# Kernel optimization log

Measured on AMD Instinct MI355X. Metric: run time of the kernel, lower is better.

The kernel has to match this reference:

```python
import jax, jax.numpy as jnp
import numpy as np

EPS = 0.1
MAX_ITER = 100
THRESH = 0.1


def _M(C, u, v):
    # M_ij = (-C_ij + u_i + v_j) / eps  -> [B, N, Mp]
    return (-C + u[..., :, None] + v[..., None, :]) / EPS


def setup_inputs() -> dict:
    key = jax.random.key(0)
    k1, k2, k3 = jax.random.split(key, 3)
    x = jax.random.normal(k1, (16, 1024, 2), dtype=jnp.float32)
    y = jax.random.normal(k2, (16, 1024, 2), dtype=jnp.float32)
    C = jax.random.uniform(k3, (16, 1024, 1024), dtype=jnp.float32)
    return {"x": x, "y": y, "C": C}


def _sinkhorn(x, y, C):
    B = x.shape[0]
    N = x.shape[-2]
    Mp = y.shape[-2]
    mu = jnp.full((B, N), 1.0 / N, dtype=jnp.float32)
    nu = jnp.full((B, Mp), 1.0 / Mp, dtype=jnp.float32)
    log_mu = jnp.log(mu + 1e-8)
    log_nu = jnp.log(nu + 1e-8)

    u0 = jnp.zeros_like(mu)
    v0 = jnp.zeros_like(nu)

    def body(carry, _):
        u, v, done = carry
        u1 = u
        u_new = EPS * (log_mu - jax.nn.logsumexp(_M(C, u, v), axis=-1)) + u
        v_new = EPS * (log_nu - jax.nn.logsumexp(_M(C, u_new, v), axis=-2)) + v
        err = jnp.abs(u_new - u1).sum(-1).mean()
        # emulate torch's early break: freeze u,v once converged
        u = jnp.where(done, u, u_new)
        v = jnp.where(done, v, v_new)
        done = done | (err < THRESH)
        return (u, v, done), None

    (u, v, _), _ = jax.lax.scan(body, (u0, v0, jnp.array(False)), None, length=MAX_ITER)
    pi = jnp.exp(_M(C, u, v))                 # [B, N, Mp]
    cost = jnp.sum(pi * C, axis=(-2, -1))      # [B]
    return cost, pi


def reference(x, y, C):
    cost, pi = _sinkhorn(x, y, C)
    return (cost, pi, C)
```

## Files before the change

### kernel.cpp

```cpp
#include <hip/hip_runtime.h>
#include <hip/hip_fp16.h>

#define BB 16
#define NN 1024
#define MAX_ITER 100

constexpr float EPS_F    = 0.1f;
constexpr float INV_EPS  = 10.0f;
constexpr float MU_P     = 0.0009765625f + 1e-8f;
constexpr float LOG_MU   = -6.9314615656526045f;
constexpr float THRESH_B = 1.6f;

#define SCOPE_AGENT __HIP_MEMORY_SCOPE_AGENT

__device__ __forceinline__ float coh_loadf(float* p) {
    return __hip_atomic_load(p, __ATOMIC_RELAXED, SCOPE_AGENT);
}
__device__ __forceinline__ int coh_loadi(int* p) {
    return __hip_atomic_load(p, __ATOMIC_RELAXED, SCOPE_AGENT);
}
__device__ __forceinline__ void coh_storef(float* p, float v) {
    atomicExch(p, v);
}

__device__ __forceinline__ void batch_sync(int* cnt, int target) {
    __syncthreads();
    if (threadIdx.x == 0) {
        __threadfence_block();
        atomicAdd(cnt, 1);
        while (coh_loadi(cnt) < target) __builtin_amdgcn_s_sleep(1);
        __threadfence_block();
    }
    __syncthreads();
}

__global__ __launch_bounds__(256) void prep_kernel(
    const float* __restrict__ C, __half* __restrict__ E,
    float* __restrict__ u, float* __restrict__ wv,
    float* __restrict__ errB, float* __restrict__ errTot,
    int* __restrict__ errCnt, int* __restrict__ bsync)
{
    size_t gid = (size_t)blockIdx.x * 256 + threadIdx.x;
    float4 c = ((const float4*)C)[gid];
    __half2* E2 = (__half2*)E;
    E2[2*gid]   = __floats2half2_rn(__expf(-INV_EPS*c.x), __expf(-INV_EPS*c.y));
    E2[2*gid+1] = __floats2half2_rn(__expf(-INV_EPS*c.z), __expf(-INV_EPS*c.w));
    if (gid < BB*NN) { u[gid] = 0.f; wv[gid] = 1.f; }
    if (gid < 6400) errB[gid] = 0.f;
    if (gid < 400)  { errTot[gid] = 0.f; errCnt[gid] = 0; }
    if (gid < 256)  bsync[gid] = 0;
}

__global__ __launch_bounds__(1024, 4) void sink_iter(
    const __half* __restrict__ E, float* __restrict__ u, float* __restrict__ v,
    float* __restrict__ wv, float* __restrict__ Tpart,
    float* __restrict__ errB, float* __restrict__ errTot,
    int* __restrict__ errCnt, int* __restrict__ bsync)
{
    const int tid  = threadIdx.x;
    const int lane = tid & 63;
    const int wav  = tid >> 6;
    const int blk  = blockIdx.x;
    const int slot = blk >> 3;
    const int b    = ((blk & 7) << 1) | (slot >> 4);
    const int sub  = slot & 15;

    const __half* Eb = E + ((size_t)b << 20);
    float* ub  = u  + (b << 10);
    float* vb  = v  + (b << 10);
    float* wvb = wv + (b << 10);
    float* Tb  = Tpart + (b << 14);
    int*   bs  = bsync + (b << 4);

    __shared__ float part[16][1028];
    __shared__ float wv_lds[1024];
    __shared__ float werr[16];
    __shared__ float errv_s;

    for (int it = 0; it < MAX_ITER; ++it) {
        wv_lds[tid ^ (((tid >> 4) & 7) << 2)] = coh_loadf(&wvb[tid]);
        __syncthreads();

        float wf[16];
        #pragma unroll
        for (int j = 0; j < 4; ++j) {
            int idx = ((lane << 4) | (j << 2)) ^ ((lane & 7) << 2);
            float4 t4 = *(const float4*)&wv_lds[idx];
            wf[4*j+0] = t4.x; wf[4*j+1] = t4.y; wf[4*j+2] = t4.z; wf[4*j+3] = t4.w;
        }

        float acc[16];
        #pragma unroll
        for (int k = 0; k < 16; ++k) acc[k] = 0.f;
        float derr = 0.f;
        #pragma unroll
        for (int r = 0; r < 4; ++r) {
            const int row = (sub << 6) + (wav << 2) + r;
            const uint4* Ep = (const uint4*)(Eb + ((size_t)row << 10));
            union { uint4 q; __half2 h[4]; } a0, a1;
            a0.q = Ep[2*lane];
            a1.q = Ep[2*lane + 1];
            float f0[8], f1[8];
            #pragma unroll
            for (int k = 0; k < 4; ++k) {
                float2 fa = __half22float2(a0.h[k]);
                float2 fb = __half22float2(a1.h[k]);
                f0[2*k] = fa.x; f0[2*k+1] = fa.y;
                f1[2*k] = fb.x; f1[2*k+1] = fb.y;
            }
            float s = 0.f;
            #pragma unroll
            for (int k = 0; k < 8; ++k) s = fmaf(f0[k], wf[k], s);
            #pragma unroll
            for (int k = 0; k < 8; ++k) s = fmaf(f1[k], wf[8+k], s);
            #pragma unroll
            for (int off = 32; off >= 1; off >>= 1) s += __shfl_xor(s, off);
            float un = EPS_F * (LOG_MU - __logf(s));
            derr += fabsf(un - ub[row]);
            if (lane == 0) ub[row] = un;
            float wuv = MU_P / s;
            #pragma unroll
            for (int k = 0; k < 8; ++k) acc[k]   = fmaf(f0[k], wuv, acc[k]);
            #pragma unroll
            for (int k = 0; k < 8; ++k) acc[8+k] = fmaf(f1[k], wuv, acc[8+k]);
        }
        if (lane == 0) werr[wav] = derr;

        #pragma unroll
        for (int j = 0; j < 4; ++j) {
            int idx = ((lane << 4) | (j << 2)) ^ ((lane & 7) << 2);
            *(float4*)&part[wav][idx] =
                make_float4(acc[4*j], acc[4*j+1], acc[4*j+2], acc[4*j+3]);
        }
        __syncthreads();

        {
            int pidx = tid ^ (((tid >> 4) & 7) << 2);
            float ts = 0.f;
            #pragma unroll
            for (int w = 0; w < 16; ++w) ts += part[w][pidx];
            coh_storef(&Tb[(sub << 10) + tid], ts);
        }
        if (wav == 0) {
            float e = (lane < 16) ? werr[lane] : 0.f;
            #pragma unroll
            for (int off = 8; off >= 1; off >>= 1) e += __shfl_xor(e, off);
            if (lane == 0) atomicAdd(&errB[(((it << 4) + b) << 2)], e);
        }

        batch_sync(bs, (it << 5) + 16);

        if (sub == 0 && tid == 0) {
            float eb = coh_loadf(&errB[(((it << 4) + b) << 2)]);
            atomicAdd(&errTot[it << 2], eb);
            __threadfence_block();
            atomicAdd(&errCnt[it << 2], 1);
        }

        {
            const int s16 = tid >> 6;
            const int cl  = tid & 63;
            float pv = coh_loadf(&Tb[(s16 << 10) + (sub << 6) + cl]);
            part[s16][cl] = pv;
            __syncthreads();
            if (tid < 64) {
                float t = 0.f;
                #pragma unroll
                for (int w = 0; w < 16; ++w) t += part[w][tid];
                const int col = (sub << 6) + tid;
                vb[col] = EPS_F * (LOG_MU - __logf(t));
                coh_storef(&wvb[col], MU_P / t);
            }
        }

        batch_sync(bs, (it << 5) + 32);

        if (tid == 0) {
            while (coh_loadi(&errCnt[it << 2]) < 16) __builtin_amdgcn_s_sleep(1);
            errv_s = coh_loadf(&errTot[it << 2]);
        }
        __syncthreads();
        if (errv_s < THRESH_B) break;
    }
}

__global__ __launch_bounds__(256) void epilogue(
    const float* __restrict__ C, const float* __restrict__ u, const float* __restrict__ v,
    float* __restrict__ outPi, float* __restrict__ outC, float* __restrict__ part)
{
    int blk = blockIdx.x;
    int b = blk >> 10;
    int i = blk & 1023;
    size_t base = (size_t)blk << 10;
    const float4* C4 = (const float4*)(C + base);
    const float4* v4 = (const float4*)(v + ((size_t)b << 10));
    float4* P4 = (float4*)(outPi + base);
    float4* O4 = (float4*)(outC + base);
    float ui = u[(b << 10) + i];
    int t = threadIdx.x;
    float4 c = C4[t];
    float4 vv = v4[t];
    float4 p;
    p.x = __expf((ui + vv.x - c.x) * INV_EPS);
    p.y = __expf((ui + vv.y - c.y) * INV_EPS);
    p.z = __expf((ui + vv.z - c.z) * INV_EPS);
    p.w = __expf((ui + vv.w - c.w) * INV_EPS);
    P4[t] = p;
    O4[t] = c;
    float cp = p.x*c.x + p.y*c.y + p.z*c.z + p.w*c.w;
    #pragma unroll
    for (int off = 32; off >= 1; off >>= 1) cp += __shfl_xor(cp, off);
    __shared__ float ps[4];
    if ((t & 63) == 0) ps[t >> 6] = cp;
    __syncthreads();
    if (t == 0) part[blk] = ps[0] + ps[1] + ps[2] + ps[3];
}

__global__ __launch_bounds__(1024) void cost_reduce(
    const float* __restrict__ part, float* __restrict__ outCost)
{
    int b = blockIdx.x;
    int t = threadIdx.x;
    float s = part[(b << 10) + t];
    #pragma unroll
    for (int off = 32; off >= 1; off >>= 1) s += __shfl_xor(s, off);
    __shared__ float ps[16];
    if ((t & 63) == 0) ps[t >> 6] = s;
    __syncthreads();
    if (t < 64) {
        float e = (t < 16) ? ps[t] : 0.f;
        #pragma unroll
        for (int off = 8; off >= 1; off >>= 1) e += __shfl_xor(e, off);
        if (t == 0) outCost[b] = e;
    }
}

extern "C" void kernel_launch(void* const* d_in, const int* in_sizes, int n_in,
                              void* d_out, int out_size, void* d_ws, size_t ws_size,
                              hipStream_t stream)
{
    const float* C = (const float*)d_in[2];
    float* out = (float*)d_out;

    char* ws = (char*)d_ws;
    __half* E     = (__half*)ws;
    float* u      = (float*)(ws + (size_t)33554432);
    float* v      = u + 16384;
    float* wv     = v + 16384;
    float* part   = wv + 16384;
    float* errB   = part + 16384;
    float* errTot = errB + 6400;
    int*   errCnt = (int*)(errTot + 400);
    int*   bsync  = errCnt + 400;

    float* outPi = out + 16;
    float* outC  = out + 16 + (size_t)16777216;
    float* Tpart = outPi;

    prep_kernel<<<16384, 256, 0, stream>>>(C, E, u, wv, errB, errTot, errCnt, bsync);

    void* args[] = { (void*)&E, (void*)&u, (void*)&v, (void*)&wv, (void*)&Tpart,
                     (void*)&errB, (void*)&errTot, (void*)&errCnt, (void*)&bsync };
    hipLaunchCooperativeKernel((void*)sink_iter, dim3(256), dim3(1024),
                               args, 0, stream);

    epilogue<<<16384, 256, 0, stream>>>(C, u, v, outPi, outC, part);
    cost_reduce<<<16, 1024, 0, stream>>>(part, out);
}
```

Before: 253.7 us.

## Keep exp(-C/eps) tiles in registers and merge v-update into one barrier

Removes the prep kernel that wrote a half-precision exp(-C/eps) matrix to workspace. Each block now computes its own tile from C once and keeps it in registers across all iterations, so the loop no longer streams E from memory. The v update is made redundant per block: every block reads all 16 partial column sums from a double-buffered Tpart and computes wv locally, which drops the second grid barrier and the wv round-trip. u is kept in registers and written back only at the end, and the cost reduction kernel is replaced by atomics in the epilogue. The costs are higher register pressure, redundant reads of Tpart by every block, and a non-deterministic atomic summation order for the cost.

```diff
diff --git a/kernel.cpp b/kernel.cpp
--- a/kernel.cpp
+++ b/kernel.cpp
@@ -26,34 +26,23 @@
 __device__ __forceinline__ void batch_sync(int* cnt, int target) {
     __syncthreads();
     if (threadIdx.x == 0) {
-        __threadfence_block();
         atomicAdd(cnt, 1);
         while (coh_loadi(cnt) < target) __builtin_amdgcn_s_sleep(1);
-        __threadfence_block();
     }
     __syncthreads();
 }
 
-__global__ __launch_bounds__(256) void prep_kernel(
-    const float* __restrict__ C, __half* __restrict__ E,
-    float* __restrict__ u, float* __restrict__ wv,
-    float* __restrict__ errB, float* __restrict__ errTot,
-    int* __restrict__ errCnt, int* __restrict__ bsync)
-{
-    size_t gid = (size_t)blockIdx.x * 256 + threadIdx.x;
-    float4 c = ((const float4*)C)[gid];
-    __half2* E2 = (__half2*)E;
-    E2[2*gid]   = __floats2half2_rn(__expf(-INV_EPS*c.x), __expf(-INV_EPS*c.y));
-    E2[2*gid+1] = __floats2half2_rn(__expf(-INV_EPS*c.z), __expf(-INV_EPS*c.w));
-    if (gid < BB*NN) { u[gid] = 0.f; wv[gid] = 1.f; }
-    if (gid < 6400) errB[gid] = 0.f;
-    if (gid < 400)  { errTot[gid] = 0.f; errCnt[gid] = 0; }
-    if (gid < 256)  bsync[gid] = 0;
+__global__ __launch_bounds__(1024) void init_kernel(
+    int* __restrict__ ctrs, float* __restrict__ outCost)
+{
+    int gid = blockIdx.x * 1024 + threadIdx.x;
+    if (gid < 7456) ctrs[gid] = 0;
+    if (gid < BB)   outCost[gid] = 0.f;
 }
 
 __global__ __launch_bounds__(1024, 4) void sink_iter(
-    const __half* __restrict__ E, float* __restrict__ u, float* __restrict__ v,
-    float* __restrict__ wv, float* __restrict__ Tpart,
+    const float* __restrict__ C, float* __restrict__ u, float* __restrict__ v,
+    float* __restrict__ Tpart,
     float* __restrict__ errB, float* __restrict__ errTot,
     int* __restrict__ errCnt, int* __restrict__ bsync)
 {
@@ -65,11 +54,10 @@
     const int b    = ((blk & 7) << 1) | (slot >> 4);
     const int sub  = slot & 15;
 
-    const __half* Eb = E + ((size_t)b << 20);
-    float* ub  = u  + (b << 10);
-    float* vb  = v  + (b << 10);
-    float* wvb = wv + (b << 10);
-    float* Tb  = Tpart + (b << 14);
+    const float* Cb = C + ((size_t)b << 20);
+    float* ub  = u + (b << 10);
+    float* vb  = v + (b << 10);
+    float* Tb  = Tpart + (b << 15);
     int*   bs  = bsync + (b << 4);
 
     __shared__ float part[16][1028];
@@ -77,9 +65,32 @@
     __shared__ float werr[16];
     __shared__ float errv_s;
 
+    uint4 e[4][2];
+    #pragma unroll
+    for (int r = 0; r < 4; ++r) {
+        const float4* C4 = (const float4*)(
+            Cb + (((size_t)((sub << 6) + (wav << 2) + r)) << 10) + (lane << 4));
+        float4 c0 = C4[0], c1 = C4[1], c2 = C4[2], c3 = C4[3];
+        union { uint4 q; __half2 h[4]; } p0, p1;
+        p0.h[0] = __floats2half2_rn(__expf(-INV_EPS*c0.x), __expf(-INV_EPS*c0.y));
+        p0.h[1] = __floats2half2_rn(__expf(-INV_EPS*c0.z), __expf(-INV_EPS*c0.w));
+        p0.h[2] = __floats2half2_rn(__expf(-INV_EPS*c1.x), __expf(-INV_EPS*c1.y));
+        p0.h[3] = __floats2half2_rn(__expf(-INV_EPS*c1.z), __expf(-INV_EPS*c1.w));
+        p1.h[0] = __floats2half2_rn(__expf(-INV_EPS*c2.x), __expf(-INV_EPS*c2.y));
+        p1.h[1] = __floats2half2_rn(__expf(-INV_EPS*c2.z), __expf(-INV_EPS*c2.w));
+        p1.h[2] = __floats2half2_rn(__expf(-INV_EPS*c3.x), __expf(-INV_EPS*c3.y));
+        p1.h[3] = __floats2half2_rn(__expf(-INV_EPS*c3.z), __expf(-INV_EPS*c3.w));
+        e[r][0] = p0.q;
+        e[r][1] = p1.q;
+    }
+
+    float u_prev[4] = {0.f, 0.f, 0.f, 0.f};
+    float t_last = 1.0f;
+    wv_lds[tid] = 1.0f;
+    __syncthreads();
+
     for (int it = 0; it < MAX_ITER; ++it) {
-        wv_lds[tid ^ (((tid >> 4) & 7) << 2)] = coh_loadf(&wvb[tid]);
-        __syncthreads();
+        const int par = it & 1;
 
         float wf[16];
         #pragma unroll
@@ -95,34 +106,27 @@
         float derr = 0.f;
         #pragma unroll
         for (int r = 0; r < 4; ++r) {
-            const int row = (sub << 6) + (wav << 2) + r;
-            const uint4* Ep = (const uint4*)(Eb + ((size_t)row << 10));
             union { uint4 q; __half2 h[4]; } a0, a1;
-            a0.q = Ep[2*lane];
-            a1.q = Ep[2*lane + 1];
-            float f0[8], f1[8];
+            a0.q = e[r][0]; a1.q = e[r][1];
+            float f[16];
             #pragma unroll
             for (int k = 0; k < 4; ++k) {
                 float2 fa = __half22float2(a0.h[k]);
                 float2 fb = __half22float2(a1.h[k]);
-                f0[2*k] = fa.x; f0[2*k+1] = fa.y;
-                f1[2*k] = fb.x; f1[2*k+1] = fb.y;
+                f[2*k]   = fa.x; f[2*k+1]   = fa.y;
+                f[8+2*k] = fb.x; f[8+2*k+1] = fb.y;
             }
             float s = 0.f;
             #pragma unroll
-            for (int k = 0; k < 8; ++k) s = fmaf(f0[k], wf[k], s);
-            #pragma unroll
-            for (int k = 0; k < 8; ++k) s = fmaf(f1[k], wf[8+k], s);
+            for (int k = 0; k < 16; ++k) s = fmaf(f[k], wf[k], s);
             #pragma unroll
             for (int off = 32; off >= 1; off >>= 1) s += __shfl_xor(s, off);
             float un = EPS_F * (LOG_MU - __logf(s));
-            derr += fabsf(un - ub[row]);
-            if (lane == 0) ub[row] = un;
+            derr += fabsf(un - u_prev[r]);
+            u_prev[r] = un;
             float wuv = MU_P / s;
             #pragma unroll
-            for (int k = 0; k < 8; ++k) acc[k]   = fmaf(f0[k], wuv, acc[k]);
-            #pragma unroll
-            for (int k = 0; k < 8; ++k) acc[8+k] = fmaf(f1[k], wuv, acc[8+k]);
+            for (int k = 0; k < 16; ++k) acc[k] = fmaf(f[k], wuv, acc[k]);
         }
         if (lane == 0) werr[wav] = derr;
 
@@ -139,41 +143,34 @@
             float ts = 0.f;
             #pragma unroll
             for (int w = 0; w < 16; ++w) ts += part[w][pidx];
-            coh_storef(&Tb[(sub << 10) + tid], ts);
+            coh_storef(&Tb[(par << 14) | (sub << 10) | tid], ts);
         }
         if (wav == 0) {
-            float e = (lane < 16) ? werr[lane] : 0.f;
-            #pragma unroll
-            for (int off = 8; off >= 1; off >>= 1) e += __shfl_xor(e, off);
-            if (lane == 0) atomicAdd(&errB[(((it << 4) + b) << 2)], e);
-        }
-
-        batch_sync(bs, (it << 5) + 16);
+            float ev = (lane < 16) ? werr[lane] : 0.f;
+            #pragma unroll
+            for (int off = 8; off >= 1; off >>= 1) ev += __shfl_xor(ev, off);
+            if (lane == 0) atomicAdd(&errB[(((it << 4) + b) << 2)], ev);
+        }
+
+        batch_sync(bs, (it + 1) << 4);
 
         if (sub == 0 && tid == 0) {
             float eb = coh_loadf(&errB[(((it << 4) + b) << 2)]);
             atomicAdd(&errTot[it << 2], eb);
-            __threadfence_block();
+            __threadfence();
             atomicAdd(&errCnt[it << 2], 1);
         }
 
         {
-            const int s16 = tid >> 6;
-            const int cl  = tid & 63;
-            float pv = coh_loadf(&Tb[(s16 << 10) + (sub << 6) + cl]);
-            part[s16][cl] = pv;
-            __syncthreads();
-            if (tid < 64) {
-                float t = 0.f;
-                #pragma unroll
-                for (int w = 0; w < 16; ++w) t += part[w][tid];
-                const int col = (sub << 6) + tid;
-                vb[col] = EPS_F * (LOG_MU - __logf(t));
-                coh_storef(&wvb[col], MU_P / t);
-            }
-        }
-
-        batch_sync(bs, (it << 5) + 32);
+            float* Tp = Tb + (par << 14);
+            float t = 0.f;
+            #pragma unroll
+            for (int s16 = 0; s16 < 16; ++s16)
+                t += coh_loadf(&Tp[(s16 << 10) | tid]);
+            t_last = t;
+            wv_lds[tid ^ (((tid >> 4) & 7) << 2)] = MU_P / t;
+        }
+        __syncthreads();
 
         if (tid == 0) {
             while (coh_loadi(&errCnt[it << 2]) < 16) __builtin_amdgcn_s_sleep(1);
@@ -182,11 +179,17 @@
         __syncthreads();
         if (errv_s < THRESH_B) break;
     }
+
+    #pragma unroll
+    for (int r = 0; r < 4; ++r)
+        if (lane == 0) ub[(sub << 6) + (wav << 2) + r] = u_prev[r];
+    if ((tid >> 6) == sub)
+        vb[tid] = EPS_F * (LOG_MU - __logf(t_last));
 }
 
 __global__ __launch_bounds__(256) void epilogue(
     const float* __restrict__ C, const float* __restrict__ u, const float* __restrict__ v,
-    float* __restrict__ outPi, float* __restrict__ outC, float* __restrict__ part)
+    float* __restrict__ outPi, float* __restrict__ outC, float* __restrict__ outCost)
 {
     int blk = blockIdx.x;
     int b = blk >> 10;
@@ -213,26 +216,7 @@
     __shared__ float ps[4];
     if ((t & 63) == 0) ps[t >> 6] = cp;
     __syncthreads();
-    if (t == 0) part[blk] = ps[0] + ps[1] + ps[2] + ps[3];
-}
-
-__global__ __launch_bounds__(1024) void cost_reduce(
-    const float* __restrict__ part, float* __restrict__ outCost)
-{
-    int b = blockIdx.x;
-    int t = threadIdx.x;
-    float s = part[(b << 10) + t];
-    #pragma unroll
-    for (int off = 32; off >= 1; off >>= 1) s += __shfl_xor(s, off);
-    __shared__ float ps[16];
-    if ((t & 63) == 0) ps[t >> 6] = s;
-    __syncthreads();
-    if (t < 64) {
-        float e = (t < 16) ? ps[t] : 0.f;
-        #pragma unroll
-        for (int off = 8; off >= 1; off >>= 1) e += __shfl_xor(e, off);
-        if (t == 0) outCost[b] = e;
-    }
+    if (t == 0) atomicAdd(&outCost[b], ps[0] + ps[1] + ps[2] + ps[3]);
 }
 
 extern "C" void kernel_launch(void* const* d_in, const int* in_sizes, int n_in,
@@ -242,28 +226,23 @@
     const float* C = (const float*)d_in[2];
     float* out = (float*)d_out;
 
-    char* ws = (char*)d_ws;
-    __half* E     = (__half*)ws;
-    float* u      = (float*)(ws + (size_t)33554432);
+    float* u      = (float*)d_ws;
     float* v      = u + 16384;
-    float* wv     = v + 16384;
-    float* part   = wv + 16384;
-    float* errB   = part + 16384;
+    float* Tpart  = v + 16384;
+    float* errB   = Tpart + 524288;
     float* errTot = errB + 6400;
     int*   errCnt = (int*)(errTot + 400);
     int*   bsync  = errCnt + 400;
 
     float* outPi = out + 16;
     float* outC  = out + 16 + (size_t)16777216;
-    float* Tpart = outPi;
-
-    prep_kernel<<<16384, 256, 0, stream>>>(C, E, u, wv, errB, errTot, errCnt, bsync);
-
-    void* args[] = { (void*)&E, (void*)&u, (void*)&v, (void*)&wv, (void*)&Tpart,
+
+    init_kernel<<<8, 1024, 0, stream>>>((int*)errB, out);
+
+    void* args[] = { (void*)&C, (void*)&u, (void*)&v, (void*)&Tpart,
                      (void*)&errB, (void*)&errTot, (void*)&errCnt, (void*)&bsync };
     hipLaunchCooperativeKernel((void*)sink_iter, dim3(256), dim3(1024),
                                args, 0, stream);
 
-    epilogue<<<16384, 256, 0, stream>>>(C, u, v, outPi, outC, part);
-    cost_reduce<<<16, 1024, 0, stream>>>(part, out);
-}
+    epilogue<<<16384, 256, 0, stream>>>(C, u, v, outPi, outC, out);
+}
```

Result: slower. 423.6 us (+67.0%).
